# Performance work log

Hardware: AMD Instinct MI355X
Metric: run time of the kernel (lower is better)

## Reference

```python
import jax, jax.numpy as jnp
import numpy as np

R_BLOCKS = 64
BLOCK_SIZE = 64
N_ELEMENTS = BLOCK_SIZE * (BLOCK_SIZE - 1) // 2  # 2016
NUM_NEUMANN_TERMS = 5

# strict upper-triangle indices (constants)
_TRIU_ROWS, _TRIU_COLS = np.triu_indices(BLOCK_SIZE, k=1)


def skew_symmetric(vec):
    # vec: (r, n_elements) -> (r, block, block) skew-symmetric
    r = vec.shape[0]
    m = jnp.zeros((r, BLOCK_SIZE, BLOCK_SIZE), dtype=vec.dtype)
    m = m.at[:, _TRIU_ROWS, _TRIU_COLS].set(vec)
    return m - jnp.swapaxes(m, -2, -1)


def cayley_neumann(weight):
    # R = I + 2Q + 2Q^2 + ... (truncated Neumann series of (I+Q)(I-Q)^-1)
    Q = skew_symmetric(weight)                     # (r, b, b)
    I = jnp.eye(BLOCK_SIZE, dtype=weight.dtype)
    R = jnp.broadcast_to(I, Q.shape) + 2.0 * Q
    Q_sq = jnp.matmul(Q, Q)
    R = R + 2.0 * Q_sq
    Q_pow = Q_sq
    for _ in range(3, NUM_NEUMANN_TERMS):
        Q_pow = jnp.matmul(Q_pow, Q)
        R = R + 2.0 * Q_pow
    return R


def setup_inputs() -> dict:
    key = jax.random.key(0)
    k1, k2 = jax.random.split(key)
    x = jax.random.normal(k1, (4, 4096, R_BLOCKS * BLOCK_SIZE), dtype=jnp.float32)
    weight = jax.random.normal(k2, (R_BLOCKS, N_ELEMENTS), dtype=jnp.float32) * 0.02
    return {"x": x, "weight": weight}


def reference(x, weight):
    rot = cayley_neumann(weight)                   # (r, block, block)
    B, S, D = x.shape
    x_r = x.reshape(B, S, R_BLOCKS, BLOCK_SIZE)    # (B, S, r, k)
    y = jnp.einsum('bsrk,rkc->bsrc', x_r, rot)
    return y.reshape(B, S, D)
```

## Files before the change

### kernel.cpp

```cpp
#include <hip/hip_runtime.h>
#include <hip/hip_bf16.h>

typedef __bf16 bf16x8 __attribute__((ext_vector_type(8)));
typedef float  f32x4  __attribute__((ext_vector_type(4)));

#define BS 64
#define RB 64
#define NELEM 2016
#define DD 4096
#define MROWS 16384
#define TILES 8

__global__ __launch_bounds__(256) void rot_kernel(const float* __restrict__ w,
                                                  __bf16* __restrict__ Rpk) {
    const int blk = blockIdx.x;
    const int t   = threadIdx.x;
    __shared__ float Q [BS * BS];
    __shared__ float B0[BS * BS];
    __shared__ float B1[BS * BS];
    const float* wb = w + blk * NELEM;

    for (int e = t; e < BS * BS; e += 256) {
        const int i = e >> 6, j = e & 63;
        float v = 0.f;
        if (i < j)      v =  wb[63 * i - (i * (i - 1)) / 2 + (j - i - 1)];
        else if (i > j) v = -wb[63 * j - (j * (j - 1)) / 2 + (i - j - 1)];
        Q[e] = v;
    }
    __syncthreads();

    const int j     = t & 63;
    const int ibase = (t >> 6) << 4;

    float qcol[BS];
#pragma unroll
    for (int k = 0; k < BS; ++k) qcol[k] = Q[k * BS + j];

    float racc[16];
#pragma unroll
    for (int s = 0; s < 16; ++s) {
        const int i = ibase + s;
        racc[s] = (i == j ? 1.f : 0.f) + 2.f * Q[i * BS + j];
    }

    const float* P = Q;
    float*       T = B0;
    for (int pass = 0; pass < 3; ++pass) {
#pragma unroll
        for (int s = 0; s < 16; ++s) {
            const int i = ibase + s;
            float sum = 0.f;
#pragma unroll
            for (int k = 0; k < BS; ++k) sum += P[i * BS + k] * qcol[k];
            T[i * BS + j] = sum;
            racc[s] += 2.f * sum;
        }
        __syncthreads();
        P = T;
        T = (pass == 0) ? B1 : B0;
    }

#pragma unroll
    for (int s = 0; s < 16; ++s) {
        const int i  = ibase + s;
        const int kf = i >> 5;
        const int g  = (i >> 3) & 3;
        const int jj = i & 7;
        const int lane = 16 * g + (j & 15);
        const int n    = j >> 4;
        Rpk[(size_t)((blk * 8 + kf * 4 + n) * 64 + lane) * 8 + jj] = (__bf16)racc[s];
    }
}

__global__ __launch_bounds__(256) void apply_kernel(const float* __restrict__ x,
                                                    const __bf16* __restrict__ Rpk,
                                                    float* __restrict__ y) {
    const int tid  = threadIdx.x;
    const int l    = tid & 63;
    const int W    = blockIdx.x * 4 + (tid >> 6);
    const int rblk = W & 63;
    const int rg   = W >> 6;
    const int g    = l >> 4;
    const int c    = l & 15;

    bf16x8 bfrag[2][4];
    const bf16x8* rp = reinterpret_cast<const bf16x8*>(Rpk) + (size_t)rblk * 8 * 64 + l;
#pragma unroll
    for (int kf = 0; kf < 2; ++kf)
#pragma unroll
        for (int n = 0; n < 4; ++n)
            bfrag[kf][n] = rp[(kf * 4 + n) * 64];

    const long rowbase = (long)rg * (TILES * 16);
    const float* xlane = x + (rowbase + (l & 15)) * (long)DD + rblk * 64 + g * 8;

    const f32x4 zero = {0.f, 0.f, 0.f, 0.f};

    f32x4 v[4], vn[4];
#pragma unroll
    for (int q = 0; q < 4; ++q)
        v[q] = *reinterpret_cast<const f32x4*>(xlane + (q >> 1) * 32 + (q & 1) * 4);

#pragma unroll
    for (int t = 0; t < TILES; ++t) {
        if (t + 1 < TILES) {
            const float* xp = xlane + (long)(t + 1) * 16 * DD;
#pragma unroll
            for (int q = 0; q < 4; ++q)
                vn[q] = *reinterpret_cast<const f32x4*>(xp + (q >> 1) * 32 + (q & 1) * 4);
        }

        bf16x8 a0, a1;
#pragma unroll
        for (int e = 0; e < 4; ++e) {
            a0[e]     = (__bf16)v[0][e];
            a0[e + 4] = (__bf16)v[1][e];
            a1[e]     = (__bf16)v[2][e];
            a1[e + 4] = (__bf16)v[3][e];
        }

        f32x4 acc[4];
#pragma unroll
        for (int n = 0; n < 4; ++n)
            acc[n] = __builtin_amdgcn_mfma_f32_16x16x32_bf16(a0, bfrag[0][n], zero, 0, 0, 0);
#pragma unroll
        for (int n = 0; n < 4; ++n)
            acc[n] = __builtin_amdgcn_mfma_f32_16x16x32_bf16(a1, bfrag[1][n], acc[n], 0, 0, 0);

        float* yl = y + (rowbase + t * 16 + 4 * g) * (long)DD + rblk * 64 + c;
#pragma unroll
        for (int n = 0; n < 4; ++n)
#pragma unroll
            for (int i = 0; i < 4; ++i)
                __builtin_nontemporal_store(acc[n][i], yl + (long)i * DD + n * 16);

#pragma unroll
        for (int q = 0; q < 4; ++q) v[q] = vn[q];
    }
}

extern "C" void kernel_launch(void* const* d_in, const int* in_sizes, int n_in,
                              void* d_out, int out_size, void* d_ws, size_t ws_size,
                              hipStream_t stream) {
    (void)in_sizes; (void)n_in; (void)out_size; (void)ws_size;
    const float* x = (const float*)d_in[0];
    const float* w = (const float*)d_in[1];
    float* y = (float*)d_out;
    __bf16* Rpk = (__bf16*)d_ws;

    rot_kernel<<<RB, 256, 0, stream>>>(w, Rpk);

    const int waves  = RB * (MROWS / (TILES * 16));
    const int blocks = waves / 4;
    apply_kernel<<<blocks, 256, 0, stream>>>(x, Rpk, y);
}
```

Measured before the change: 124.4 us.

## Split rotation-matrix computation across four blocks per rotation block by row slab

```diff
diff --git a/kernel.cpp b/kernel.cpp
--- a/kernel.cpp
+++ b/kernel.cpp
@@ -13,11 +13,13 @@
 
 __global__ __launch_bounds__(256) void rot_kernel(const float* __restrict__ w,
                                                   __bf16* __restrict__ Rpk) {
-    const int blk = blockIdx.x;
-    const int t   = threadIdx.x;
+    const int bid   = blockIdx.x;
+    const int blk   = bid >> 2;
+    const int rbase = (bid & 3) * 16;
+    const int t     = threadIdx.x;
     __shared__ float Q [BS * BS];
-    __shared__ float B0[BS * BS];
-    __shared__ float B1[BS * BS];
+    __shared__ float T0[16 * BS];
+    __shared__ float T1[16 * BS];
     const float* wb = w + blk * NELEM;
 
     for (int e = t; e < BS * BS; e += 256) {
@@ -29,40 +31,54 @@
     }
     __syncthreads();
 
-    const int j     = t & 63;
-    const int ibase = (t >> 6) << 4;
+    const int j  = t & 63;
+    const int s4 = (t >> 6) * 4;
 
     float qcol[BS];
 #pragma unroll
     for (int k = 0; k < BS; ++k) qcol[k] = Q[k * BS + j];
 
-    float racc[16];
+    float racc[4];
 #pragma unroll
-    for (int s = 0; s < 16; ++s) {
-        const int i = ibase + s;
+    for (int s = 0; s < 4; ++s) {
+        const int i = rbase + s4 + s;
         racc[s] = (i == j ? 1.f : 0.f) + 2.f * Q[i * BS + j];
     }
 
-    const float* P = Q;
-    float*       T = B0;
-    for (int pass = 0; pass < 3; ++pass) {
 #pragma unroll
-        for (int s = 0; s < 16; ++s) {
-            const int i = ibase + s;
-            float sum = 0.f;
+    for (int s = 0; s < 4; ++s) {
+        const int i = rbase + s4 + s;
+        float sum = 0.f;
 #pragma unroll
-            for (int k = 0; k < BS; ++k) sum += P[i * BS + k] * qcol[k];
-            T[i * BS + j] = sum;
-            racc[s] += 2.f * sum;
-        }
-        __syncthreads();
-        P = T;
-        T = (pass == 0) ? B1 : B0;
+        for (int k = 0; k < BS; ++k) sum += Q[i * BS + k] * qcol[k];
+        T0[(s4 + s) * BS + j] = sum;
+        racc[s] += 2.f * sum;
+    }
+    __syncthreads();
+
+#pragma unroll
+    for (int s = 0; s < 4; ++s) {
+        const int r = s4 + s;
+        float sum = 0.f;
+#pragma unroll
+        for (int k = 0; k < BS; ++k) sum += T0[r * BS + k] * qcol[k];
+        T1[r * BS + j] = sum;
+        racc[s] += 2.f * sum;
+    }
+    __syncthreads();
+
+#pragma unroll
+    for (int s = 0; s < 4; ++s) {
+        const int r = s4 + s;
+        float sum = 0.f;
+#pragma unroll
+        for (int k = 0; k < BS; ++k) sum += T1[r * BS + k] * qcol[k];
+        racc[s] += 2.f * sum;
     }
 
 #pragma unroll
-    for (int s = 0; s < 16; ++s) {
-        const int i  = ibase + s;
+    for (int s = 0; s < 4; ++s) {
+        const int i  = rbase + s4 + s;
         const int kf = i >> 5;
         const int g  = (i >> 3) & 3;
         const int jj = i & 7;
@@ -134,8 +150,10 @@
             for (int i = 0; i < 4; ++i)
                 __builtin_nontemporal_store(acc[n][i], yl + (long)i * DD + n * 16);
 
+        if (t + 1 < TILES) {
 #pragma unroll
-        for (int q = 0; q < 4; ++q) v[q] = vn[q];
+            for (int q = 0; q < 4; ++q) v[q] = vn[q];
+        }
     }
 }
 
@@ -148,7 +166,7 @@
     float* y = (float*)d_out;
     __bf16* Rpk = (__bf16*)d_ws;
 
-    rot_kernel<<<RB, 256, 0, stream>>>(w, Rpk);
+    rot_kernel<<<RB * 4, 256, 0, stream>>>(w, Rpk);
 
     const int waves  = RB * (MROWS / (TILES * 16));
     const int blocks = waves / 4;
```

Result: faster. 117.9 us, median of 2 (-5.2%).
